# Optimization experiments

Measured on AMD Instinct MI355X. Metric: run time of the kernel, lower is better.

## Reference

```python
import jax, jax.numpy as jnp
import numpy as np

D = 16       # data dimension
M = 64       # hidden width
ALPHA0 = 1.0 # alpha[0]
H_RES = 1.0  # ResNet step h = 1/(n_layers-1), n_layers=2


def _antideriv_tanh(x):
    # log(exp(x)+exp(-x)), numerically stable
    return jnp.abs(x) + jnp.log1p(jnp.exp(-2.0 * jnp.abs(x)))


def _dtanh(x):
    t = jnp.tanh(x)
    return 1.0 - t * t


def grad_and_hessian_trace(s, w, A, b, K0, b0, K1, b1):
    """OT-Flow analytic grad of Phi and trace of Hessian (w.r.t. first d coords).
    s: (n, d+1) = [x; t]. n_layers=2 -> one residual layer, h=1."""
    d = s.shape[1] - 1
    opening = s @ K0.T + b0                         # (n, m)
    u0 = _antideriv_tanh(opening)                   # (n, m)
    feat1 = u0 @ K1.T + b1                          # (n, m)
    tanhopen = jnp.tanh(opening)                    # (n, m)
    # backward pass for gradient: z1 = w + h K1^T (tanh(feat1) * w)
    z1 = w + H_RES * (jnp.tanh(feat1) * w) @ K1     # (n, m)
    z0 = (tanhopen * z1) @ K0                       # (n, d+1)
    symA = A.T @ A                                  # (d+1, d+1)
    grad = z0 + s @ symA + b                        # (n, d+1)
    # Hessian trace: opening-layer term
    Kopen = K0[:, :d]                               # (m, d)
    trH = (_dtanh(opening) * z1) @ jnp.sum(Kopen**2, axis=1)   # (n,)
    # forward-propagated Jacobian of u0 w.r.t. x: (n, m, d)
    Jac = tanhopen[:, :, None] * Kopen[None, :, :]
    KJ = jnp.einsum('ij,njd->nid', K1, Jac)         # (n, m, d)
    t1 = jnp.einsum('nm,nmd->n', _dtanh(feat1) * w, KJ**2)
    trH = trH + H_RES * t1 + jnp.sum(A[:, :d] ** 2)  # + trace(symA[:d,:d])
    return grad, trH


def odefun(z, t, w, A, b, K0, b0, K1, b1):
    n = z.shape[0]
    x = z[:, :D]
    s = jnp.concatenate([x, jnp.full((n, 1), t, dtype=z.dtype)], axis=1)
    gradPhi, trH = grad_and_hessian_trace(s, w, A, b, K0, b0, K1, b1)
    dx = -(1.0 / ALPHA0) * gradPhi[:, :D]
    dl = -(1.0 / ALPHA0) * trH[:, None]
    dv = 0.5 * jnp.sum(dx * dx, axis=1, keepdims=True)
    dr = jnp.abs(-gradPhi[:, -1:] + ALPHA0 * dv)
    return jnp.concatenate([dx, dl, dv, dr], axis=1)


def step_rk4(f, z, t0, t1):
    h = t1 - t0
    z0 = z
    K = h * f(z0, t0)
    z = z0 + K / 6.0
    K = h * f(z0 + 0.5 * K, t0 + 0.5 * h)
    z = z + K / 3.0
    K = h * f(z0 + 0.5 * K, t0 + 0.5 * h)
    z = z + K / 3.0
    K = h * f(z0 + K, t0 + h)
    z = z + K / 6.0
    return z


def setup_inputs() -> dict:
    key = jax.random.key(0)
    ks = jax.random.split(key, 8)
    n = 32768
    dp1 = D + 1
    x = jax.random.normal(ks[0], (n, D), dtype=jnp.float32)
    w = jax.random.normal(ks[1], (M,), dtype=jnp.float32) / np.sqrt(M)
    A = 0.1 * jax.random.normal(ks[2], (10, dp1), dtype=jnp.float32)
    b = 0.1 * jax.random.normal(ks[3], (dp1,), dtype=jnp.float32)
    K0 = jax.random.normal(ks[4], (M, dp1), dtype=jnp.float32) / np.sqrt(dp1)
    b0 = 0.1 * jax.random.normal(ks[5], (M,), dtype=jnp.float32)
    K1 = jax.random.normal(ks[6], (M, M), dtype=jnp.float32) / np.sqrt(M)
    b1 = 0.1 * jax.random.normal(ks[7], (M,), dtype=jnp.float32)
    return {"x": x, "w": w, "A": A, "b": b, "K0": K0, "b0": b0,
            "K1": K1, "b1": b1, "nt": 8}


def reference(x, w, A, b, K0, b0, K1, b1, nt):
    f = lambda z, t: odefun(z, t, w, A, b, K0, b0, K1, b1)
    h = 1.0 / nt
    z = jnp.concatenate([x, jnp.zeros((x.shape[0], 3), x.dtype)], axis=1)
    for k in range(nt):  # nt is a static python int
        z = step_rk4(f, z, k * h, (k + 1) * h)
    # unpack: (x_latent, log_det, transport_cost, hjb_violation)
    return z[:, :D], z[:, D], z[:, D + 1], z[:, D + 2]
```

## Files before the change

### kernel.cpp

```cpp
#include <hip/hip_runtime.h>
#include <math.h>

typedef __attribute__((ext_vector_type(8))) short bf16x8;
typedef __attribute__((ext_vector_type(4))) float f32x4;

union B8 { bf16x8 v; unsigned u[4]; };

__device__ __forceinline__ unsigned pk2(float lo, float hi) {
  unsigned r;
  asm("v_cvt_pk_bf16_f32 %0, %1, %2" : "=v"(r) : "v"(lo), "v"(hi));
  return r;
}
__device__ __forceinline__ float rcpf(float x) { return __builtin_amdgcn_rcpf(x); }
__device__ __forceinline__ void ldsfence() { asm volatile("s_waitcnt lgkmcnt(0)" ::: "memory"); }

#define MFMA __builtin_amdgcn_mfma_f32_16x16x32_bf16

__global__ void otflow_prep(const float* __restrict__ K0g,
                            const float* __restrict__ Ag,
                            float* __restrict__ ws) {
  __shared__ float Als[170];
  int tid = threadIdx.x;
  for (int idx = tid; idx < 1024; idx += 256) {
    int m = idx >> 4, d = idx & 15;
    ws[idx] = K0g[m * 17 + d];
  }
  if (tid < 170) Als[tid] = Ag[tid];
  if (tid < 64) {
    float s = 0.f;
    for (int d = 0; d < 16; ++d) { float v = K0g[tid * 17 + d]; s += v * v; }
    ws[1320 + tid] = s;
  }
  __syncthreads();
  for (int idx = tid; idx < 289; idx += 256) {
    int j = idx / 17, k2 = idx % 17;
    float s = 0.f;
#pragma unroll
    for (int r = 0; r < 10; ++r) s += Als[r * 17 + j] * Als[r * 17 + k2];
    ws[1024 + idx] = s;
  }
  __syncthreads();
  if (tid == 0) {
    float s = 0.f;
    for (int r = 0; r < 10; ++r)
      for (int j = 0; j < 16; ++j) { float v = Als[r * 17 + j]; s += v * v; }
    ws[1313] = s;
  }
}

__global__ __launch_bounds__(64, 2) void otflow_main(
    const float* __restrict__ xg, const float* __restrict__ wg,
    const float* __restrict__ bg, const float* __restrict__ K0g,
    const float* __restrict__ b0g, const float* __restrict__ K1g,
    const float* __restrict__ b1g, const int* __restrict__ ntg,
    const float* __restrict__ ws, float* __restrict__ out, int n) {
  __shared__ float buf[16 * 68];
  __shared__ float csh[16 * 68];
  __shared__ float qsh[16 * 68];
  __shared__ float tsh[16 * 20];
  __shared__ float b1s[64], wss[64], k0qs[64], b0s[64], tcs[64];

  const int lane = threadIdx.x;
  const int lr = lane & 15;
  const int lg = lane >> 4;

  b1s[lane] = b1g[lane];
  wss[lane] = wg[lane];
  k0qs[lane] = ws[1320 + lane];
  b0s[lane] = b0g[lane];
  tcs[lane] = K0g[lane * 17 + 16];

  const float sumA2 = ws[1313];

  B8 aK0[4], aK0L[4], aK1[8], aK1T[8], aG[6];
  float kop[16];
#pragma unroll
  for (int mi = 0; mi < 4; ++mi) {
    B8 th, tl;
#pragma unroll
    for (int jj = 0; jj < 4; ++jj) {
      float e0 = K0g[(mi * 16 + lr) * 17 + (lg & 1) * 8 + jj * 2];
      float e1 = K0g[(mi * 16 + lr) * 17 + (lg & 1) * 8 + jj * 2 + 1];
      unsigned hh = pk2(e0, e1);
      th.u[jj] = hh;
      float l0 = e0 - __uint_as_float(hh << 16);
      float l1 = e1 - __uint_as_float(hh & 0xffff0000u);
      tl.u[jj] = pk2(l0, l1);
    }
    aK0[mi] = th; aK0L[mi] = tl;
  }
#pragma unroll
  for (int mi = 0; mi < 4; ++mi)
#pragma unroll
    for (int kb = 0; kb < 2; ++kb) {
      const float* pp = K1g + (mi * 16 + lr) * 64 + kb * 32 + lg * 8;
      float4 q0 = *(const float4*)pp;
      float4 q1 = *(const float4*)(pp + 4);
      B8 t;
      t.u[0] = pk2(q0.x, q0.y); t.u[1] = pk2(q0.z, q0.w);
      t.u[2] = pk2(q1.x, q1.y); t.u[3] = pk2(q1.z, q1.w);
      aK1[mi * 2 + kb] = t;
    }
#pragma unroll
  for (int mi = 0; mi < 4; ++mi)
#pragma unroll
    for (int kb = 0; kb < 2; ++kb) {
      int ib = kb * 32 + lg * 8;
      int m = mi * 16 + lr;
      B8 t;
#pragma unroll
      for (int jj = 0; jj < 4; ++jj)
        t.u[jj] = pk2(K1g[(ib + jj * 2) * 64 + m], K1g[(ib + jj * 2 + 1) * 64 + m]);
      aK1T[mi * 2 + kb] = t;
    }
#pragma unroll
  for (int nb = 0; nb < 2; ++nb)
#pragma unroll
    for (int kb = 0; kb < 3; ++kb) {
      int j = nb * 16 + lr; if (j > 16) j = 16;
      float e[8];
#pragma unroll
      for (int jj = 0; jj < 8; ++jj) {
        float v;
        if (kb < 2) v = K0g[(kb * 32 + lg * 8 + jj) * 17 + j];
        else {
          int kr = lg * 8 + jj;
          v = (kr < 17) ? ws[1024 + kr * 17 + j] : (kr == 17) ? bg[j] : 0.f;
        }
        e[jj] = v;
      }
      B8 t;
      t.u[0] = pk2(e[0], e[1]); t.u[1] = pk2(e[2], e[3]);
      t.u[2] = pk2(e[4], e[5]); t.u[3] = pk2(e[6], e[7]);
      aG[nb * 3 + kb] = t;
    }
#pragma unroll
  for (int kb = 0; kb < 2; ++kb)
#pragma unroll
    for (int j = 0; j < 8; ++j)
      kop[kb * 8 + j] = ws[(kb * 32 + lg * 8 + j) * 16 + lr];

  ldsfence();

  const int nt = *ntg;
  const float h = 1.0f / (float)nt;
  const int p0 = blockIdx.x * 16;
  int pidx = p0 + lr; if (pidx >= n) pidx = n - 1;

  float xin[4], x0s[4], xac[4];
  {
    float4 xi = *(const float4*)(xg + (size_t)pidx * 16 + lg * 4);
    xin[0] = xi.x; xin[1] = xi.y; xin[2] = xi.z; xin[3] = xi.w;
#pragma unroll
    for (int r = 0; r < 4; ++r) { x0s[r] = xin[r]; xac[r] = xin[r]; }
  }
  float lacc = 0.f, vacc = 0.f, racc = 0.f;
  const f32x4 zz = {0.f, 0.f, 0.f, 0.f};

  for (int kstep = 0; kstep < nt; ++kstep) {
    float t0 = (float)kstep * h;
#pragma unroll 1
    for (int st = 0; st < 4; ++st) {
      float tin = t0 + ((st == 0) ? 0.f : (st == 3) ? h : 0.5f * h);

      { float4 xv = {xin[0], xin[1], xin[2], xin[3]};
        *(float4*)(buf + lr * 68 + lg * 4) = xv; }
      ldsfence();
      float4 s0 = *(const float4*)(buf + lr * 68 + (lg & 1) * 8);
      float4 s1 = *(const float4*)(buf + lr * 68 + (lg & 1) * 8 + 4);
      unsigned h0 = pk2(s0.x, s0.y), h1 = pk2(s0.z, s0.w);
      unsigned h2 = pk2(s1.x, s1.y), h3 = pk2(s1.z, s1.w);
      B8 sfO, sfG;
      if (lg < 2) {
        sfO.u[0] = h0; sfO.u[1] = h1; sfO.u[2] = h2; sfO.u[3] = h3;
        sfG.u[0] = h0; sfG.u[1] = h1; sfG.u[2] = h2; sfG.u[3] = h3;
      } else {
        float l0 = s0.x - __uint_as_float(h0 << 16);
        float l1 = s0.y - __uint_as_float(h0 & 0xffff0000u);
        float l2 = s0.z - __uint_as_float(h1 << 16);
        float l3 = s0.w - __uint_as_float(h1 & 0xffff0000u);
        float l4 = s1.x - __uint_as_float(h2 << 16);
        float l5 = s1.y - __uint_as_float(h2 & 0xffff0000u);
        float l6 = s1.z - __uint_as_float(h3 << 16);
        float l7 = s1.w - __uint_as_float(h3 & 0xffff0000u);
        sfO.u[0] = pk2(l0, l1); sfO.u[1] = pk2(l2, l3);
        sfO.u[2] = pk2(l4, l5); sfO.u[3] = pk2(l6, l7);
        if (lg == 2) { sfG.u[0] = pk2(tin, 1.f); sfG.u[1] = 0; sfG.u[2] = 0; sfG.u[3] = 0; }
        else { sfG.u[0] = 0; sfG.u[1] = 0; sfG.u[2] = 0; sfG.u[3] = 0; }
      }

      f32x4 o0 = MFMA(aK0[0].v, sfO.v, zz, 0, 0, 0);
      f32x4 o1 = MFMA(aK0[1].v, sfO.v, zz, 0, 0, 0);
      f32x4 o2 = MFMA(aK0[2].v, sfO.v, zz, 0, 0, 0);
      f32x4 o3 = MFMA(aK0[3].v, sfO.v, zz, 0, 0, 0);
      o0 = MFMA(aK0L[0].v, sfO.v, o0, 0, 0, 0);
      o1 = MFMA(aK0L[1].v, sfO.v, o1, 0, 0, 0);
      o2 = MFMA(aK0L[2].v, sfO.v, o2, 0, 0, 0);
      o3 = MFMA(aK0L[3].v, sfO.v, o3, 0, 0, 0);

      float cva[16];
#pragma unroll
      for (int mi = 0; mi < 4; ++mi) {
        f32x4 oa = (mi == 0) ? o0 : (mi == 1) ? o1 : (mi == 2) ? o2 : o3;
        float4 b0v = *(const float4*)(b0s + mi * 16 + lg * 4);
        float4 tcv = *(const float4*)(tcs + mi * 16 + lg * 4);
        float4 u0v;
#pragma unroll
        for (int r = 0; r < 4; ++r) {
          float ov = oa[r] + fmaf(tin, ((const float*)&tcv)[r], ((const float*)&b0v)[r]);
          float e = __expf(-2.f * fabsf(ov));
          float rp = rcpf(1.f + e);
          float cm = (1.f - e) * rp;
          cva[mi * 4 + r] = __builtin_copysignf(cm, ov);
          ((float*)&u0v)[r] = fabsf(ov) + __logf(1.f + e);
        }
        *(float4*)(buf + lr * 68 + mi * 16 + lg * 4) = u0v;
      }
      ldsfence();

      B8 uf0, uf1;
      {
        const float* bp = buf + lr * 68;
        float4 a0 = *(const float4*)(bp + lg * 8);
        float4 a1 = *(const float4*)(bp + lg * 8 + 4);
        float4 a2 = *(const float4*)(bp + 32 + lg * 8);
        float4 a3 = *(const float4*)(bp + 32 + lg * 8 + 4);
        uf0.u[0] = pk2(a0.x, a0.y); uf0.u[1] = pk2(a0.z, a0.w);
        uf0.u[2] = pk2(a1.x, a1.y); uf0.u[3] = pk2(a1.z, a1.w);
        uf1.u[0] = pk2(a2.x, a2.y); uf1.u[1] = pk2(a2.z, a2.w);
        uf1.u[2] = pk2(a3.x, a3.y); uf1.u[3] = pk2(a3.z, a3.w);
      }
      f32x4 f0 = MFMA(aK1[0].v, uf0.v, zz, 0, 0, 0); f0 = MFMA(aK1[1].v, uf1.v, f0, 0, 0, 0);
      f32x4 f1 = MFMA(aK1[2].v, uf0.v, zz, 0, 0, 0); f1 = MFMA(aK1[3].v, uf1.v, f1, 0, 0, 0);
      f32x4 f2 = MFMA(aK1[4].v, uf0.v, zz, 0, 0, 0); f2 = MFMA(aK1[5].v, uf1.v, f2, 0, 0, 0);
      f32x4 f3 = MFMA(aK1[6].v, uf0.v, zz, 0, 0, 0); f3 = MFMA(aK1[7].v, uf1.v, f3, 0, 0, 0);

#pragma unroll
      for (int mi = 0; mi < 4; ++mi) {
        f32x4 fa = (mi == 0) ? f0 : (mi == 1) ? f1 : (mi == 2) ? f2 : f3;
        float4 b1v = *(const float4*)(b1s + mi * 16 + lg * 4);
        float4 wv = *(const float4*)(wss + mi * 16 + lg * 4);
        float4 av4, qv4;
#pragma unroll
        for (int r = 0; r < 4; ++r) {
          float fv = fa[r] + ((const float*)&b1v)[r];
          float e = __expf(-2.f * fabsf(fv));
          float rp = rcpf(1.f + e);
          float tf = __builtin_copysignf((1.f - e) * rp, fv);
          float wr = ((const float*)&wv)[r];
          ((float*)&av4)[r] = tf * wr;
          ((float*)&qv4)[r] = (1.f - tf * tf) * wr;
        }
        *(float4*)(buf + lr * 68 + mi * 16 + lg * 4) = av4;
        *(float4*)(qsh + lr * 68 + mi * 16 + lg * 4) = qv4;
      }
      ldsfence();

      B8 af0, af1;
      {
        const float* bp = buf + lr * 68;
        float4 a0 = *(const float4*)(bp + lg * 8);
        float4 a1 = *(const float4*)(bp + lg * 8 + 4);
        float4 a2 = *(const float4*)(bp + 32 + lg * 8);
        float4 a3 = *(const float4*)(bp + 32 + lg * 8 + 4);
        af0.u[0] = pk2(a0.x, a0.y); af0.u[1] = pk2(a0.z, a0.w);
        af0.u[2] = pk2(a1.x, a1.y); af0.u[3] = pk2(a1.z, a1.w);
        af1.u[0] = pk2(a2.x, a2.y); af1.u[1] = pk2(a2.z, a2.w);
        af1.u[2] = pk2(a3.x, a3.y); af1.u[3] = pk2(a3.z, a3.w);
      }
      f32x4 z0 = MFMA(aK1T[0].v, af0.v, zz, 0, 0, 0); z0 = MFMA(aK1T[1].v, af1.v, z0, 0, 0, 0);
      f32x4 z1 = MFMA(aK1T[2].v, af0.v, zz, 0, 0, 0); z1 = MFMA(aK1T[3].v, af1.v, z1, 0, 0, 0);
      f32x4 z2 = MFMA(aK1T[4].v, af0.v, zz, 0, 0, 0); z2 = MFMA(aK1T[5].v, af1.v, z2, 0, 0, 0);
      f32x4 z3 = MFMA(aK1T[6].v, af0.v, zz, 0, 0, 0); z3 = MFMA(aK1T[7].v, af1.v, z3, 0, 0, 0);

      float trh_l = 0.f;
#pragma unroll
      for (int mi = 0; mi < 4; ++mi) {
        f32x4 za = (mi == 0) ? z0 : (mi == 1) ? z1 : (mi == 2) ? z2 : z3;
        float4 wv = *(const float4*)(wss + mi * 16 + lg * 4);
        float4 kq = *(const float4*)(k0qs + mi * 16 + lg * 4);
        float4 rv4, cv4;
#pragma unroll
        for (int r = 0; r < 4; ++r) {
          float c = cva[mi * 4 + r];
          float z1v = za[r] + ((const float*)&wv)[r];
          ((float*)&rv4)[r] = c * z1v;
          float dt0 = 1.f - c * c;
          trh_l = fmaf(dt0 * z1v, ((const float*)&kq)[r], trh_l);
          ((float*)&cv4)[r] = c;
        }
        *(float4*)(buf + lr * 68 + mi * 16 + lg * 4) = rv4;
        *(float4*)(csh + lr * 68 + mi * 16 + lg * 4) = cv4;
      }
      trh_l += __shfl_xor(trh_l, 16, 64);
      trh_l += __shfl_xor(trh_l, 32, 64);
      ldsfence();

#pragma unroll 2
      for (int p = 0; p < 16; ++p) {
        const float* cp = csh + p * 68;
        float4 ca = *(const float4*)(cp + lg * 8);
        float4 cb = *(const float4*)(cp + lg * 8 + 4);
        float4 cc = *(const float4*)(cp + 32 + lg * 8);
        float4 cd = *(const float4*)(cp + 32 + lg * 8 + 4);
        B8 y0, y1;
        y0.u[0] = pk2(ca.x * kop[0], ca.y * kop[1]);
        y0.u[1] = pk2(ca.z * kop[2], ca.w * kop[3]);
        y0.u[2] = pk2(cb.x * kop[4], cb.y * kop[5]);
        y0.u[3] = pk2(cb.z * kop[6], cb.w * kop[7]);
        y1.u[0] = pk2(cc.x * kop[8], cc.y * kop[9]);
        y1.u[1] = pk2(cc.z * kop[10], cc.w * kop[11]);
        y1.u[2] = pk2(cd.x * kop[12], cd.y * kop[13]);
        y1.u[3] = pk2(cd.z * kop[14], cd.w * kop[15]);
        f32x4 kc0 = MFMA(y0.v, aK1[0].v, zz, 0, 0, 0); kc0 = MFMA(y1.v, aK1[1].v, kc0, 0, 0, 0);
        f32x4 kc1 = MFMA(y0.v, aK1[2].v, zz, 0, 0, 0); kc1 = MFMA(y1.v, aK1[3].v, kc1, 0, 0, 0);
        f32x4 kc2 = MFMA(y0.v, aK1[4].v, zz, 0, 0, 0); kc2 = MFMA(y1.v, aK1[5].v, kc2, 0, 0, 0);
        f32x4 kc3 = MFMA(y0.v, aK1[6].v, zz, 0, 0, 0); kc3 = MFMA(y1.v, aK1[7].v, kc3, 0, 0, 0);
        float q0 = qsh[p * 68 + lr];
        float q1 = qsh[p * 68 + 16 + lr];
        float q2 = qsh[p * 68 + 32 + lr];
        float q3 = qsh[p * 68 + 48 + lr];
        float d0 = kc0[0] * kc0[0] + kc0[1] * kc0[1] + kc0[2] * kc0[2] + kc0[3] * kc0[3];
        float d1 = kc1[0] * kc1[0] + kc1[1] * kc1[1] + kc1[2] * kc1[2] + kc1[3] * kc1[3];
        float d2 = kc2[0] * kc2[0] + kc2[1] * kc2[1] + kc2[2] * kc2[2] + kc2[3] * kc2[3];
        float d3 = kc3[0] * kc3[0] + kc3[1] * kc3[1] + kc3[2] * kc3[2] + kc3[3] * kc3[3];
        float tp = q0 * d0 + q1 * d1 + q2 * d2 + q3 * d3;
        tp += __shfl_xor(tp, 16, 64);
        tp += __shfl_xor(tp, 32, 64);
        if (lg == 0) tsh[p * 20 + lr] = tp;
      }
      ldsfence();
      float4 tv = *(const float4*)(tsh + lr * 20 + lg * 4);
      float tsum = tv.x + tv.y + tv.z + tv.w;
      tsum += __shfl_xor(tsum, 16, 64);
      tsum += __shfl_xor(tsum, 32, 64);

      B8 rf0, rf1;
      {
        const float* bp = buf + lr * 68;
        float4 a0 = *(const float4*)(bp + lg * 8);
        float4 a1 = *(const float4*)(bp + lg * 8 + 4);
        float4 a2 = *(const float4*)(bp + 32 + lg * 8);
        float4 a3 = *(const float4*)(bp + 32 + lg * 8 + 4);
        rf0.u[0] = pk2(a0.x, a0.y); rf0.u[1] = pk2(a0.z, a0.w);
        rf0.u[2] = pk2(a1.x, a1.y); rf0.u[3] = pk2(a1.z, a1.w);
        rf1.u[0] = pk2(a2.x, a2.y); rf1.u[1] = pk2(a2.z, a2.w);
        rf1.u[2] = pk2(a3.x, a3.y); rf1.u[3] = pk2(a3.z, a3.w);
      }
      f32x4 g0 = MFMA(aG[0].v, rf0.v, zz, 0, 0, 0);
      g0 = MFMA(aG[1].v, rf1.v, g0, 0, 0, 0);
      g0 = MFMA(aG[2].v, sfG.v, g0, 0, 0, 0);
      f32x4 g1 = MFMA(aG[3].v, rf0.v, zz, 0, 0, 0);
      g1 = MFMA(aG[4].v, rf1.v, g1, 0, 0, 0);
      g1 = MFMA(aG[5].v, sfG.v, g1, 0, 0, 0);

      float kx[4];
      float dvp = 0.f;
#pragma unroll
      for (int r = 0; r < 4; ++r) { float d = -g0[r]; kx[r] = d; dvp = fmaf(d, d, dvp); }
      dvp += __shfl_xor(dvp, 16, 64);
      dvp += __shfl_xor(dvp, 32, 64);
      dvp *= 0.5f;
      float g16 = g1[0];
      float trH = trh_l + tsum + sumA2;
      float dl = -trH;
      float dr = fabsf(dvp - g16);
      float wch = ((st == 0 || st == 3) ? (1.f / 6.f) : (1.f / 3.f)) * h;
#pragma unroll
      for (int r = 0; r < 4; ++r) xac[r] = fmaf(wch, kx[r], xac[r]);
      lacc = fmaf(wch, dl, lacc);
      vacc = fmaf(wch, dvp, vacc);
      racc = fmaf(wch, dr, racc);
      if (st < 3) {
        float anh = ((st == 2) ? 1.f : 0.5f) * h;
#pragma unroll
        for (int r = 0; r < 4; ++r) xin[r] = fmaf(anh, kx[r], x0s[r]);
      } else {
#pragma unroll
        for (int r = 0; r < 4; ++r) { x0s[r] = xac[r]; xin[r] = xac[r]; }
      }
    }
  }

  if (p0 + lr < n) {
    float4 xa = {xac[0], xac[1], xac[2], xac[3]};
    *(float4*)(out + (size_t)(p0 + lr) * 16 + lg * 4) = xa;
    if (lg == 0) {
      out[(size_t)n * 16 + p0 + lr] = lacc;
      out[(size_t)n * 17 + p0 + lr] = vacc;
      out[(size_t)n * 18 + p0 + lr] = racc;
    }
  }
}

extern "C" void kernel_launch(void* const* d_in, const int* in_sizes, int n_in,
                              void* d_out, int out_size, void* d_ws, size_t ws_size,
                              hipStream_t stream) {
  const float* xg = (const float*)d_in[0];
  const float* wg = (const float*)d_in[1];
  const float* Ag = (const float*)d_in[2];
  const float* bg = (const float*)d_in[3];
  const float* K0g = (const float*)d_in[4];
  const float* b0g = (const float*)d_in[5];
  const float* K1g = (const float*)d_in[6];
  const float* b1g = (const float*)d_in[7];
  const int* ntg = (const int*)d_in[8];
  float* out = (float*)d_out;
  float* ws = (float*)d_ws;
  int n = in_sizes[0] / 16;

  hipLaunchKernelGGL(otflow_prep, dim3(1), dim3(256), 0, stream, K0g, Ag, ws);
  int nblk = (n + 15) / 16;
  hipLaunchKernelGGL(otflow_main, dim3(nblk), dim3(64), 0, stream,
                     xg, wg, bg, K0g, b0g, K1g, b1g, ntg, ws, out, n);
}
```

Measured before the change: 358.3 us.

## Stage bf16-packed MFMA operands in LDS and compute time-gradient column on VALU

Intermediate activations are now converted to bf16 once and written packed into a dedicated LDS buffer, so the next MFMA reads ready operands with a single 128-bit load instead of reloading fp32 values and repacking them. The tanh values are written to csh during the opening layer rather than in a later pass. The gradient's time column (g16) is computed with scalar FMAs and shuffles, which removes the second set of three gradient MFMAs and frees their registers. The kop scaling uses packed fp32 multiplies, and the gradient MFMA is moved ahead of the LDS fence so it can overlap the trace reduction. The time column is now formed from fp32 values rather than bf16, which changes rounding slightly.

```diff
diff --git a/kernel.cpp b/kernel.cpp
--- a/kernel.cpp
+++ b/kernel.cpp
@@ -3,12 +3,19 @@
 
 typedef __attribute__((ext_vector_type(8))) short bf16x8;
 typedef __attribute__((ext_vector_type(4))) float f32x4;
-
-union B8 { bf16x8 v; unsigned u[4]; };
+typedef __attribute__((ext_vector_type(2))) float f32x2;
+typedef __attribute__((ext_vector_type(4))) unsigned u32x4;
+
+union B8 { bf16x8 v; unsigned u[4]; u32x4 q; };
 
 __device__ __forceinline__ unsigned pk2(float lo, float hi) {
   unsigned r;
   asm("v_cvt_pk_bf16_f32 %0, %1, %2" : "=v"(r) : "v"(lo), "v"(hi));
+  return r;
+}
+__device__ __forceinline__ f32x2 pkmul(f32x2 a, f32x2 b) {
+  f32x2 r;
+  asm("v_pk_mul_f32 %0, %1, %2" : "=v"(r) : "v"(a), "v"(b));
   return r;
 }
 __device__ __forceinline__ float rcpf(float x) { return __builtin_amdgcn_rcpf(x); }
@@ -54,26 +61,28 @@
     const float* __restrict__ b0g, const float* __restrict__ K1g,
     const float* __restrict__ b1g, const int* __restrict__ ntg,
     const float* __restrict__ ws, float* __restrict__ out, int n) {
-  __shared__ float buf[16 * 68];
-  __shared__ float csh[16 * 68];
-  __shared__ float qsh[16 * 68];
-  __shared__ float tsh[16 * 20];
-  __shared__ float b1s[64], wss[64], k0qs[64], b0s[64], tcs[64];
+  __shared__ __align__(16) float csh[16 * 68];
+  __shared__ __align__(16) float qsh[16 * 68];
+  __shared__ __align__(16) unsigned Xu[16 * 36];
+  __shared__ __align__(16) float tsh[16 * 20];
+  __shared__ __align__(16) float b0s[64], tcs[64], b1s[64], wss[64], k0qs[64];
+  __shared__ __align__(16) float scol[20];
 
   const int lane = threadIdx.x;
   const int lr = lane & 15;
   const int lg = lane >> 4;
 
+  b0s[lane] = b0g[lane];
+  tcs[lane] = K0g[lane * 17 + 16];
   b1s[lane] = b1g[lane];
   wss[lane] = wg[lane];
   k0qs[lane] = ws[1320 + lane];
-  b0s[lane] = b0g[lane];
-  tcs[lane] = K0g[lane * 17 + 16];
+  if (lane < 17) scol[lane] = ws[1024 + lane * 17 + 16];
+  if (lane == 17) scol[17] = bg[16];
 
   const float sumA2 = ws[1313];
 
-  B8 aK0[4], aK0L[4], aK1[8], aK1T[8], aG[6];
-  float kop[16];
+  B8 aK0[4], aK0L[4];
 #pragma unroll
   for (int mi = 0; mi < 4; ++mi) {
     B8 th, tl;
@@ -89,6 +98,7 @@
     }
     aK0[mi] = th; aK0L[mi] = tl;
   }
+  B8 aK1[8];
 #pragma unroll
   for (int mi = 0; mi < 4; ++mi)
 #pragma unroll
@@ -101,23 +111,24 @@
       t.u[2] = pk2(q1.x, q1.y); t.u[3] = pk2(q1.z, q1.w);
       aK1[mi * 2 + kb] = t;
     }
+  B8 aK1T[8];
 #pragma unroll
   for (int mi = 0; mi < 4; ++mi)
 #pragma unroll
     for (int kb = 0; kb < 2; ++kb) {
       int ib = kb * 32 + lg * 8;
       int m = mi * 16 + lr;
-      B8 t;
+      B8 tt;
 #pragma unroll
       for (int jj = 0; jj < 4; ++jj)
-        t.u[jj] = pk2(K1g[(ib + jj * 2) * 64 + m], K1g[(ib + jj * 2 + 1) * 64 + m]);
-      aK1T[mi * 2 + kb] = t;
-    }
-#pragma unroll
-  for (int nb = 0; nb < 2; ++nb)
+        tt.u[jj] = pk2(K1g[(ib + jj * 2) * 64 + m], K1g[(ib + jj * 2 + 1) * 64 + m]);
+      aK1T[mi * 2 + kb] = tt;
+    }
+  B8 aG0[3];
+  {
+    int j = lr;
 #pragma unroll
     for (int kb = 0; kb < 3; ++kb) {
-      int j = nb * 16 + lr; if (j > 16) j = 16;
       float e[8];
 #pragma unroll
       for (int jj = 0; jj < 8; ++jj) {
@@ -132,15 +143,24 @@
       B8 t;
       t.u[0] = pk2(e[0], e[1]); t.u[1] = pk2(e[2], e[3]);
       t.u[2] = pk2(e[4], e[5]); t.u[3] = pk2(e[6], e[7]);
-      aG[nb * 3 + kb] = t;
-    }
+      aG0[kb] = t;
+    }
+  }
+  f32x2 kop2[8];
 #pragma unroll
   for (int kb = 0; kb < 2; ++kb)
 #pragma unroll
-    for (int j = 0; j < 8; ++j)
-      kop[kb * 8 + j] = ws[(kb * 32 + lg * 8 + j) * 16 + lr];
+    for (int j = 0; j < 4; ++j) {
+      f32x2 t;
+      t.x = ws[(kb * 32 + lg * 8 + 2 * j) * 16 + lr];
+      t.y = ws[(kb * 32 + lg * 8 + 2 * j + 1) * 16 + lr];
+      kop2[kb * 4 + j] = t;
+    }
 
   ldsfence();
+
+  float4 sc4 = *(const float4*)(scol + lg * 4);
+  const float sc16 = scol[16], sc17 = scol[17];
 
   const int nt = *ntg;
   const float h = 1.0f / (float)nt;
@@ -164,10 +184,10 @@
       float tin = t0 + ((st == 0) ? 0.f : (st == 3) ? h : 0.5f * h);
 
       { float4 xv = {xin[0], xin[1], xin[2], xin[3]};
-        *(float4*)(buf + lr * 68 + lg * 4) = xv; }
+        *(float4*)(csh + lr * 68 + lg * 4) = xv; }
       ldsfence();
-      float4 s0 = *(const float4*)(buf + lr * 68 + (lg & 1) * 8);
-      float4 s1 = *(const float4*)(buf + lr * 68 + (lg & 1) * 8 + 4);
+      float4 s0 = *(const float4*)(csh + lr * 68 + (lg & 1) * 8);
+      float4 s1 = *(const float4*)(csh + lr * 68 + (lg & 1) * 8 + 4);
       unsigned h0 = pk2(s0.x, s0.y), h1 = pk2(s0.z, s0.w);
       unsigned h2 = pk2(s1.x, s1.y), h3 = pk2(s1.z, s1.w);
       B8 sfO, sfG;
@@ -204,32 +224,27 @@
         f32x4 oa = (mi == 0) ? o0 : (mi == 1) ? o1 : (mi == 2) ? o2 : o3;
         float4 b0v = *(const float4*)(b0s + mi * 16 + lg * 4);
         float4 tcv = *(const float4*)(tcs + mi * 16 + lg * 4);
-        float4 u0v;
+        float u0v[4];
+        float4 cv4;
 #pragma unroll
         for (int r = 0; r < 4; ++r) {
           float ov = oa[r] + fmaf(tin, ((const float*)&tcv)[r], ((const float*)&b0v)[r]);
           float e = __expf(-2.f * fabsf(ov));
           float rp = rcpf(1.f + e);
-          float cm = (1.f - e) * rp;
-          cva[mi * 4 + r] = __builtin_copysignf(cm, ov);
-          ((float*)&u0v)[r] = fabsf(ov) + __logf(1.f + e);
+          float c = __builtin_copysignf((1.f - e) * rp, ov);
+          cva[mi * 4 + r] = c;
+          u0v[r] = fabsf(ov) + __logf(1.f + e);
+          ((float*)&cv4)[r] = c;
         }
-        *(float4*)(buf + lr * 68 + mi * 16 + lg * 4) = u0v;
+        *(float4*)(csh + lr * 68 + mi * 16 + lg * 4) = cv4;
+        *(uint2*)(Xu + lr * 36 + mi * 8 + lg * 2) =
+            make_uint2(pk2(u0v[0], u0v[1]), pk2(u0v[2], u0v[3]));
       }
       ldsfence();
 
       B8 uf0, uf1;
-      {
-        const float* bp = buf + lr * 68;
-        float4 a0 = *(const float4*)(bp + lg * 8);
-        float4 a1 = *(const float4*)(bp + lg * 8 + 4);
-        float4 a2 = *(const float4*)(bp + 32 + lg * 8);
-        float4 a3 = *(const float4*)(bp + 32 + lg * 8 + 4);
-        uf0.u[0] = pk2(a0.x, a0.y); uf0.u[1] = pk2(a0.z, a0.w);
-        uf0.u[2] = pk2(a1.x, a1.y); uf0.u[3] = pk2(a1.z, a1.w);
-        uf1.u[0] = pk2(a2.x, a2.y); uf1.u[1] = pk2(a2.z, a2.w);
-        uf1.u[2] = pk2(a3.x, a3.y); uf1.u[3] = pk2(a3.z, a3.w);
-      }
+      uf0.q = *(const u32x4*)(Xu + lr * 36 + lg * 4);
+      uf1.q = *(const u32x4*)(Xu + lr * 36 + 16 + lg * 4);
       f32x4 f0 = MFMA(aK1[0].v, uf0.v, zz, 0, 0, 0); f0 = MFMA(aK1[1].v, uf1.v, f0, 0, 0, 0);
       f32x4 f1 = MFMA(aK1[2].v, uf0.v, zz, 0, 0, 0); f1 = MFMA(aK1[3].v, uf1.v, f1, 0, 0, 0);
       f32x4 f2 = MFMA(aK1[4].v, uf0.v, zz, 0, 0, 0); f2 = MFMA(aK1[5].v, uf1.v, f2, 0, 0, 0);
@@ -240,7 +255,8 @@
         f32x4 fa = (mi == 0) ? f0 : (mi == 1) ? f1 : (mi == 2) ? f2 : f3;
         float4 b1v = *(const float4*)(b1s + mi * 16 + lg * 4);
         float4 wv = *(const float4*)(wss + mi * 16 + lg * 4);
-        float4 av4, qv4;
+        float av[4];
+        float4 qv4;
 #pragma unroll
         for (int r = 0; r < 4; ++r) {
           float fv = fa[r] + ((const float*)&b1v)[r];
@@ -248,52 +264,49 @@
           float rp = rcpf(1.f + e);
           float tf = __builtin_copysignf((1.f - e) * rp, fv);
           float wr = ((const float*)&wv)[r];
-          ((float*)&av4)[r] = tf * wr;
+          av[r] = tf * wr;
           ((float*)&qv4)[r] = (1.f - tf * tf) * wr;
         }
-        *(float4*)(buf + lr * 68 + mi * 16 + lg * 4) = av4;
         *(float4*)(qsh + lr * 68 + mi * 16 + lg * 4) = qv4;
+        *(uint2*)(Xu + lr * 36 + mi * 8 + lg * 2) =
+            make_uint2(pk2(av[0], av[1]), pk2(av[2], av[3]));
       }
       ldsfence();
 
       B8 af0, af1;
-      {
-        const float* bp = buf + lr * 68;
-        float4 a0 = *(const float4*)(bp + lg * 8);
-        float4 a1 = *(const float4*)(bp + lg * 8 + 4);
-        float4 a2 = *(const float4*)(bp + 32 + lg * 8);
-        float4 a3 = *(const float4*)(bp + 32 + lg * 8 + 4);
-        af0.u[0] = pk2(a0.x, a0.y); af0.u[1] = pk2(a0.z, a0.w);
-        af0.u[2] = pk2(a1.x, a1.y); af0.u[3] = pk2(a1.z, a1.w);
-        af1.u[0] = pk2(a2.x, a2.y); af1.u[1] = pk2(a2.z, a2.w);
-        af1.u[2] = pk2(a3.x, a3.y); af1.u[3] = pk2(a3.z, a3.w);
-      }
+      af0.q = *(const u32x4*)(Xu + lr * 36 + lg * 4);
+      af1.q = *(const u32x4*)(Xu + lr * 36 + 16 + lg * 4);
       f32x4 z0 = MFMA(aK1T[0].v, af0.v, zz, 0, 0, 0); z0 = MFMA(aK1T[1].v, af1.v, z0, 0, 0, 0);
       f32x4 z1 = MFMA(aK1T[2].v, af0.v, zz, 0, 0, 0); z1 = MFMA(aK1T[3].v, af1.v, z1, 0, 0, 0);
       f32x4 z2 = MFMA(aK1T[4].v, af0.v, zz, 0, 0, 0); z2 = MFMA(aK1T[5].v, af1.v, z2, 0, 0, 0);
       f32x4 z3 = MFMA(aK1T[6].v, af0.v, zz, 0, 0, 0); z3 = MFMA(aK1T[7].v, af1.v, z3, 0, 0, 0);
 
-      float trh_l = 0.f;
+      float trh_l = 0.f, g16p = 0.f;
 #pragma unroll
       for (int mi = 0; mi < 4; ++mi) {
         f32x4 za = (mi == 0) ? z0 : (mi == 1) ? z1 : (mi == 2) ? z2 : z3;
         float4 wv = *(const float4*)(wss + mi * 16 + lg * 4);
         float4 kq = *(const float4*)(k0qs + mi * 16 + lg * 4);
-        float4 rv4, cv4;
+        float4 tcv = *(const float4*)(tcs + mi * 16 + lg * 4);
+        float rv[4];
 #pragma unroll
         for (int r = 0; r < 4; ++r) {
           float c = cva[mi * 4 + r];
           float z1v = za[r] + ((const float*)&wv)[r];
-          ((float*)&rv4)[r] = c * z1v;
-          float dt0 = 1.f - c * c;
-          trh_l = fmaf(dt0 * z1v, ((const float*)&kq)[r], trh_l);
-          ((float*)&cv4)[r] = c;
+          rv[r] = c * z1v;
+          trh_l = fmaf((1.f - c * c) * z1v, ((const float*)&kq)[r], trh_l);
+          g16p = fmaf(rv[r], ((const float*)&tcv)[r], g16p);
         }
-        *(float4*)(buf + lr * 68 + mi * 16 + lg * 4) = rv4;
-        *(float4*)(csh + lr * 68 + mi * 16 + lg * 4) = cv4;
-      }
+        *(uint2*)(Xu + lr * 36 + mi * 8 + lg * 2) =
+            make_uint2(pk2(rv[0], rv[1]), pk2(rv[2], rv[3]));
+      }
+#pragma unroll
+      for (int r = 0; r < 4; ++r) g16p = fmaf(xin[r], ((const float*)&sc4)[r], g16p);
       trh_l += __shfl_xor(trh_l, 16, 64);
       trh_l += __shfl_xor(trh_l, 32, 64);
+      g16p += __shfl_xor(g16p, 16, 64);
+      g16p += __shfl_xor(g16p, 32, 64);
+      float g16 = g16p + fmaf(tin, sc16, sc17);
       ldsfence();
 
 #pragma unroll 2
@@ -304,14 +317,15 @@
         float4 cc = *(const float4*)(cp + 32 + lg * 8);
         float4 cd = *(const float4*)(cp + 32 + lg * 8 + 4);
         B8 y0, y1;
-        y0.u[0] = pk2(ca.x * kop[0], ca.y * kop[1]);
-        y0.u[1] = pk2(ca.z * kop[2], ca.w * kop[3]);
-        y0.u[2] = pk2(cb.x * kop[4], cb.y * kop[5]);
-        y0.u[3] = pk2(cb.z * kop[6], cb.w * kop[7]);
-        y1.u[0] = pk2(cc.x * kop[8], cc.y * kop[9]);
-        y1.u[1] = pk2(cc.z * kop[10], cc.w * kop[11]);
-        y1.u[2] = pk2(cd.x * kop[12], cd.y * kop[13]);
-        y1.u[3] = pk2(cd.z * kop[14], cd.w * kop[15]);
+        f32x2 pr;
+        pr = pkmul((f32x2){ca.x, ca.y}, kop2[0]); y0.u[0] = pk2(pr.x, pr.y);
+        pr = pkmul((f32x2){ca.z, ca.w}, kop2[1]); y0.u[1] = pk2(pr.x, pr.y);
+        pr = pkmul((f32x2){cb.x, cb.y}, kop2[2]); y0.u[2] = pk2(pr.x, pr.y);
+        pr = pkmul((f32x2){cb.z, cb.w}, kop2[3]); y0.u[3] = pk2(pr.x, pr.y);
+        pr = pkmul((f32x2){cc.x, cc.y}, kop2[4]); y1.u[0] = pk2(pr.x, pr.y);
+        pr = pkmul((f32x2){cc.z, cc.w}, kop2[5]); y1.u[1] = pk2(pr.x, pr.y);
+        pr = pkmul((f32x2){cd.x, cd.y}, kop2[6]); y1.u[2] = pk2(pr.x, pr.y);
+        pr = pkmul((f32x2){cd.z, cd.w}, kop2[7]); y1.u[3] = pk2(pr.x, pr.y);
         f32x4 kc0 = MFMA(y0.v, aK1[0].v, zz, 0, 0, 0); kc0 = MFMA(y1.v, aK1[1].v, kc0, 0, 0, 0);
         f32x4 kc1 = MFMA(y0.v, aK1[2].v, zz, 0, 0, 0); kc1 = MFMA(y1.v, aK1[3].v, kc1, 0, 0, 0);
         f32x4 kc2 = MFMA(y0.v, aK1[4].v, zz, 0, 0, 0); kc2 = MFMA(y1.v, aK1[5].v, kc2, 0, 0, 0);
@@ -329,31 +343,20 @@
         tp += __shfl_xor(tp, 32, 64);
         if (lg == 0) tsh[p * 20 + lr] = tp;
       }
+
+      B8 rf0, rf1;
+      rf0.q = *(const u32x4*)(Xu + lr * 36 + lg * 4);
+      rf1.q = *(const u32x4*)(Xu + lr * 36 + 16 + lg * 4);
+      f32x4 g0 = MFMA(aG0[0].v, rf0.v, zz, 0, 0, 0);
+      g0 = MFMA(aG0[1].v, rf1.v, g0, 0, 0, 0);
+      g0 = MFMA(aG0[2].v, sfG.v, g0, 0, 0, 0);
       ldsfence();
+
       float4 tv = *(const float4*)(tsh + lr * 20 + lg * 4);
       float tsum = tv.x + tv.y + tv.z + tv.w;
       tsum += __shfl_xor(tsum, 16, 64);
       tsum += __shfl_xor(tsum, 32, 64);
 
-      B8 rf0, rf1;
-      {
-        const float* bp = buf + lr * 68;
-        float4 a0 = *(const float4*)(bp + lg * 8);
-        float4 a1 = *(const float4*)(bp + lg * 8 + 4);
-        float4 a2 = *(const float4*)(bp + 32 + lg * 8);
-        float4 a3 = *(const float4*)(bp + 32 + lg * 8 + 4);
-        rf0.u[0] = pk2(a0.x, a0.y); rf0.u[1] = pk2(a0.z, a0.w);
-        rf0.u[2] = pk2(a1.x, a1.y); rf0.u[3] = pk2(a1.z, a1.w);
-        rf1.u[0] = pk2(a2.x, a2.y); rf1.u[1] = pk2(a2.z, a2.w);
-        rf1.u[2] = pk2(a3.x, a3.y); rf1.u[3] = pk2(a3.z, a3.w);
-      }
-      f32x4 g0 = MFMA(aG[0].v, rf0.v, zz, 0, 0, 0);
-      g0 = MFMA(aG[1].v, rf1.v, g0, 0, 0, 0);
-      g0 = MFMA(aG[2].v, sfG.v, g0, 0, 0, 0);
-      f32x4 g1 = MFMA(aG[3].v, rf0.v, zz, 0, 0, 0);
-      g1 = MFMA(aG[4].v, rf1.v, g1, 0, 0, 0);
-      g1 = MFMA(aG[5].v, sfG.v, g1, 0, 0, 0);
-
       float kx[4];
       float dvp = 0.f;
 #pragma unroll
@@ -361,7 +364,6 @@
       dvp += __shfl_xor(dvp, 16, 64);
       dvp += __shfl_xor(dvp, 32, 64);
       dvp *= 0.5f;
-      float g16 = g1[0];
       float trH = trh_l + tsum + sumA2;
       float dl = -trH;
       float dr = fabsf(dvp - g16);
```

Result: faster. 349.5 us (-2.4%).
